# Optimization experiments

Measured on AMD Instinct MI355X. Metric: run time of the kernel, lower is better.

## Reference

```python
import jax, jax.numpy as jnp
import numpy as np

D_MODEL = 1024
NUM_HEADS = 16
HEAD_DIM = D_MODEL // NUM_HEADS
MAX_SEQ_LEN = 2048
THETA = 10000.0
BATCH = 2
SEQ = 2048


def _rope_tables():
    inv_freq = 1.0 / (THETA ** (jnp.arange(0, HEAD_DIM, 2, dtype=jnp.float32) / HEAD_DIM))
    pos = jnp.arange(MAX_SEQ_LEN, dtype=jnp.float32)
    freqs = pos[:, None] * inv_freq[None, :]  # [max_seq, head_dim/2]
    return jnp.sin(freqs), jnp.cos(freqs)


def _apply_rope(x, sin, cos):
    # x: [b, h, s, d]; sin/cos: [s, d/2] -> broadcast over b, h
    sin = sin[None, None, :, :]
    cos = cos[None, None, :, :]
    x_even = x[..., 0::2]
    x_odd = x[..., 1::2]
    out_even = x_even * cos - x_odd * sin
    out_odd = x_even * sin + x_odd * cos
    # interleave back: stack on new last axis then flatten
    out = jnp.stack((out_even, out_odd), axis=-1)
    return out.reshape(x.shape)


def setup_inputs() -> dict:
    key = jax.random.key(0)
    ks = jax.random.split(key, 5)
    std = (2.0 / (D_MODEL + D_MODEL)) ** 0.5
    return {
        "x": jax.random.normal(ks[0], (BATCH, SEQ, D_MODEL), dtype=jnp.float32),
        "Wq": jax.random.normal(ks[1], (D_MODEL, D_MODEL), dtype=jnp.float32) * std,
        "Wk": jax.random.normal(ks[2], (D_MODEL, D_MODEL), dtype=jnp.float32) * std,
        "Wv": jax.random.normal(ks[3], (D_MODEL, D_MODEL), dtype=jnp.float32) * std,
        "Wo": jax.random.normal(ks[4], (D_MODEL, D_MODEL), dtype=jnp.float32) * std,
    }


def reference(x, Wq, Wk, Wv, Wo):
    b, s, _ = x.shape
    # projections: weight stored [out, in] as in the torch Linear
    Q = jnp.einsum('bsd,od->bso', x, Wq)
    K = jnp.einsum('bsd,od->bso', x, Wk)
    V = jnp.einsum('bsd,od->bso', x, Wv)
    # split heads -> [b, h, s, hd]
    def split(t):
        return t.reshape(b, s, NUM_HEADS, HEAD_DIM).transpose(0, 2, 1, 3)
    Q, K, V = split(Q), split(K), split(V)
    sin, cos = _rope_tables()
    sin, cos = sin[:s], cos[:s]
    Q = _apply_rope(Q, sin, cos)
    K = _apply_rope(K, sin, cos)
    scale = 1.0 / jnp.sqrt(jnp.float32(HEAD_DIM))
    scores = jnp.einsum('bhqd,bhkd->bhqk', Q, K)
    causal = jnp.tril(jnp.ones((s, s), dtype=bool))[None, None]
    scores = jnp.where(causal, scores, -jnp.inf) * scale  # -inf * scale stays -inf
    attn = jax.nn.softmax(scores, axis=-1)
    out = jnp.einsum('bhqk,bhkd->bhqd', attn, V)
    out = out.transpose(0, 2, 1, 3).reshape(b, s, D_MODEL)
    return jnp.einsum('bsd,od->bso', out, Wo)
```

## Files before the change

kernel.cpp:

```cpp
#include <hip/hip_runtime.h>
#include <math.h>

#define NHEADS 16
#define HD 64
#define SEQ 2048
#define BATCH 2
#define DM 1024
#define MTOT (BATCH*SEQ)

typedef __bf16 bf16x8 __attribute__((ext_vector_type(8)));
typedef __bf16 bf16x4 __attribute__((ext_vector_type(4)));
typedef float  f32x4  __attribute__((ext_vector_type(4)));

#define LOG2E 1.4426950408889634f

#define GLD16(gp, lp) __builtin_amdgcn_global_load_lds( \
    (const __attribute__((address_space(1))) void*)(gp), \
    (__attribute__((address_space(3))) void*)(lp), 16, 0, 0)

__global__ __launch_bounds__(256)
void cast_all(const float* __restrict__ x, const float* __restrict__ Wq,
              const float* __restrict__ Wk, const float* __restrict__ Wv,
              const float* __restrict__ Wo,
              __bf16* __restrict__ xb, __bf16* __restrict__ Wqkvb,
              __bf16* __restrict__ Wob)
{
    const size_t NX = (size_t)MTOT * DM;
    const size_t NW_ = (size_t)DM * DM;
    const size_t i = ((size_t)blockIdx.x * 256 + threadIdx.x) * 8;
    const float* src; __bf16* dst; size_t off;
    if (i < NX)               { src = x;  dst = xb;            off = i; }
    else if (i < NX + NW_)    { src = Wq; dst = Wqkvb;         off = i - NX; }
    else if (i < NX + 2*NW_)  { src = Wk; dst = Wqkvb + NW_;   off = i - NX - NW_; }
    else if (i < NX + 3*NW_)  { src = Wv; dst = Wqkvb + 2*NW_; off = i - NX - 2*NW_; }
    else                      { src = Wo; dst = Wob;           off = i - NX - 3*NW_; }
    const float4 f0 = *(const float4*)&src[off];
    const float4 f1 = *(const float4*)&src[off + 4];
    bf16x8 o;
    o[0] = (__bf16)f0.x; o[1] = (__bf16)f0.y; o[2] = (__bf16)f0.z; o[3] = (__bf16)f0.w;
    o[4] = (__bf16)f1.x; o[5] = (__bf16)f1.y; o[6] = (__bf16)f1.z; o[7] = (__bf16)f1.w;
    *(bf16x8*)&dst[off] = o;
}

template<int BM, int BN, int MODE>
__global__ __launch_bounds__(256, 3)
void gemm_mfma(const __bf16* __restrict__ A, const __bf16* __restrict__ W,
               float* __restrict__ Cf,
               __bf16* __restrict__ Qb, __bf16* __restrict__ Kb,
               __bf16* __restrict__ Vtb)
{
    constexpr int IT = BM / 32;
    constexpr int JT = BN / 32;
    __shared__ __bf16 As[BM * 64];
    __shared__ __bf16 Bs[BN * 64];

    const int tid  = threadIdx.x;
    const int lane = tid & 63;
    const int wave = tid >> 6;
    const int ll   = lane & 15;
    const int quad = lane >> 4;
    const int wm   = (wave & 1) * (BM / 2);
    const int wn   = (wave >> 1) * (BN / 2);
    const int bm   = blockIdx.x * BM;
    const int bn   = blockIdx.y * BN;

    const __bf16* Ab = A + (size_t)bm * DM;
    const __bf16* Wb = W + (size_t)bn * DM;

    f32x4 acc[IT][JT];
#pragma unroll
    for (int i = 0; i < IT; i++)
#pragma unroll
        for (int j = 0; j < JT; j++) acc[i][j] = (f32x4){0.f, 0.f, 0.f, 0.f};

    for (int k0 = 0; k0 < DM; k0 += 64) {
#pragma unroll
        for (int j = 0; j < BM / 32; j++) {
            const int t = tid + 256 * j;
            const int r = t >> 3, g = t & 7;
            GLD16(Ab + (size_t)r * DM + k0 + ((g ^ (r & 7)) * 8), &As[t * 8]);
        }
#pragma unroll
        for (int j = 0; j < BN / 32; j++) {
            const int t = tid + 256 * j;
            const int r = t >> 3, g = t & 7;
            GLD16(Wb + (size_t)r * DM + k0 + ((g ^ (r & 7)) * 8), &Bs[t * 8]);
        }
        __syncthreads();

#pragma unroll
        for (int kh = 0; kh < 2; kh++) {
            bf16x8 af[IT], bfr[JT];
#pragma unroll
            for (int i = 0; i < IT; i++) {
                const int r = wm + i*16 + ll;
                const int g = kh*4 + quad;
                af[i] = *(const bf16x8*)&As[(r*8 + (g ^ (r & 7))) * 8];
            }
#pragma unroll
            for (int j = 0; j < JT; j++) {
                const int r = wn + j*16 + ll;
                const int g = kh*4 + quad;
                bfr[j] = *(const bf16x8*)&Bs[(r*8 + (g ^ (r & 7))) * 8];
            }
#pragma unroll
            for (int i = 0; i < IT; i++)
#pragma unroll
                for (int j = 0; j < JT; j++)
                    acc[i][j] = __builtin_amdgcn_mfma_f32_16x16x32_bf16(
                        af[i], bfr[j], acc[i][j], 0, 0, 0);
        }
        __syncthreads();
    }

    if (MODE == 1) {
#pragma unroll
        for (int i = 0; i < IT; i++) {
#pragma unroll
            for (int j = 0; j < JT; j++) {
                const int gc = bn + wn + j*16 + ll;
#pragma unroll
                for (int r = 0; r < 4; r++) {
                    const int gr = bm + wm + i*16 + quad*4 + r;
                    Cf[(size_t)gr * DM + gc] = acc[i][j][r];
                }
            }
        }
    } else {
        const int which = bn >> 10;
        const int nb = bn & 1023;
#pragma unroll
        for (int i = 0; i < IT; i++) {
            const int m0 = bm + wm + i*16 + quad*4;
            const int b  = m0 >> 11;
            const int s0 = m0 & (SEQ - 1);
#pragma unroll
            for (int j = 0; j < JT; j++) {
                const int n_g = nb + wn + j*16 + ll;
                const int h = n_g >> 6, d = n_g & (HD - 1);
                if (which == 2) {
                    bf16x4 pk;
#pragma unroll
                    for (int r = 0; r < 4; r++) pk[r] = (__bf16)acc[i][j][r];
                    *(bf16x4*)&Vtb[((size_t)((b*NHEADS + h)*HD + d)) * SEQ + s0] = pk;
                } else {
                    __bf16* P = (which == 0) ? Qb : Kb;
                    const float sc = (which == 0) ? 0.125f * LOG2E : 1.0f;
                    const float inv =
                        exp2f(-(float)(d & ~1) * (13.287712379549449f / 64.0f));
                    const bool odd = (d & 1);
#pragma unroll
                    for (int r = 0; r < 4; r++) {
                        const float own = acc[i][j][r];
                        const float oth = __shfl_xor(own, 1);
                        float sn, cs;
                        __sincosf((float)(s0 + r) * inv, &sn, &cs);
                        const float xe = odd ? oth : own;
                        const float xo = odd ? own : oth;
                        const float o = odd ? (xe * sn + xo * cs)
                                            : (xe * cs - xo * sn);
                        P[((size_t)(b*NHEADS + h) * SEQ + s0 + r) * HD + d] =
                            (__bf16)(o * sc);
                    }
                }
            }
        }
    }
}

__global__ __launch_bounds__(256, 2)
void attn_mfma(const __bf16* __restrict__ Qb, const __bf16* __restrict__ Kb,
               const __bf16* __restrict__ Vtb, __bf16* __restrict__ AOb)
{
    __shared__ __align__(16) __bf16 ptB[4][16][64];
    __shared__ float comb[4][64][17];
    __shared__ float lbuf[4][64];

    const int tid  = threadIdx.x;
    const int wave = tid >> 6;
    const int lane = tid & 63;
    const int m    = lane & 15;
    const int quad = lane >> 4;
    const int bh   = blockIdx.x;
    const int b    = bh >> 4, h = bh & 15;
    const int qb   = blockIdx.z ? (SEQ/64 - 1) - (int)blockIdx.y : (int)blockIdx.y;
    const int q0   = qb * 64;

    const __bf16* Qp = Qb + (size_t)bh * SEQ * HD;
    const __bf16* Kp = Kb + (size_t)bh * SEQ * HD;
    const __bf16* Vp = Vtb + (size_t)bh * HD * SEQ;

    bf16x8 ones;
#pragma unroll
    for (int j = 0; j < 8; j++) ones[j] = (__bf16)1.0f;

    bf16x8 qf[4][2];
#pragma unroll
    for (int i = 0; i < 4; i++) {
        const __bf16* qp = Qp + (size_t)(q0 + i*16 + m) * HD + quad*8;
        qf[i][0] = *(const bf16x8*)qp;
        qf[i][1] = *(const bf16x8*)(qp + 32);
    }

    f32x4 acc[4][4];
    f32x4 l_acc[4];
#pragma unroll
    for (int i = 0; i < 4; i++) {
        l_acc[i] = (f32x4){0.f, 0.f, 0.f, 0.f};
#pragma unroll
        for (int nt = 0; nt < 4; nt++) acc[i][nt] = (f32x4){0.f, 0.f, 0.f, 0.f};
    }

    for (int t = wave; t <= qb; t += 4) {
        const int k0 = t * 64;
        const bool diag = (t == qb);

        bf16x8 kf[4][2], vf[4][2];
#pragma unroll
        for (int tk = 0; tk < 4; tk++) {
            const __bf16* kp = Kp + (size_t)(k0 + tk*16 + m) * HD + quad*8;
            kf[tk][0] = *(const bf16x8*)kp;
            kf[tk][1] = *(const bf16x8*)(kp + 32);
            const __bf16* vp = Vp + (size_t)(tk*16 + m) * SEQ + k0 + quad*8;
            vf[tk][0] = *(const bf16x8*)vp;
            vf[tk][1] = *(const bf16x8*)(vp + 32);
        }

#pragma unroll
        for (int i = 0; i < 4; i++) {
            f32x4 s[4];
#pragma unroll
            for (int tk = 0; tk < 4; tk++) {
                s[tk] = (f32x4){0.f, 0.f, 0.f, 0.f};
                s[tk] = __builtin_amdgcn_mfma_f32_16x16x32_bf16(
                    kf[tk][0], qf[i][0], s[tk], 0, 0, 0);
                s[tk] = __builtin_amdgcn_mfma_f32_16x16x32_bf16(
                    kf[tk][1], qf[i][1], s[tk], 0, 0, 0);
            }
#pragma unroll
            for (int tk = 0; tk < 4; tk++) {
                bf16x4 pk;
#pragma unroll
                for (int r = 0; r < 4; r++) {
                    float sv = s[tk][r];
                    if (diag)
                        sv = (16*tk + quad*4 + r <= 16*i + m) ? sv : -INFINITY;
                    pk[r] = (__bf16)__builtin_amdgcn_exp2f(sv);
                }
                const int Gs = (2*tk + (quad >> 1)) ^ (m & 7);
                *(bf16x4*)&ptB[wave][m][Gs*8 + (quad & 1)*4] = pk;
            }
            const bf16x8 af0 =
                *(const bf16x8*)&ptB[wave][m][(quad ^ (m & 7))*8];
            const bf16x8 af1 =
                *(const bf16x8*)&ptB[wave][m][((4 + quad) ^ (m & 7))*8];
            l_acc[i] = __builtin_amdgcn_mfma_f32_16x16x32_bf16(
                af0, ones, l_acc[i], 0, 0, 0);
            l_acc[i] = __builtin_amdgcn_mfma_f32_16x16x32_bf16(
                af1, ones, l_acc[i], 0, 0, 0);
#pragma unroll
            for (int nt = 0; nt < 4; nt++) {
                acc[i][nt] = __builtin_amdgcn_mfma_f32_16x16x32_bf16(
                    af0, vf[nt][0], acc[i][nt], 0, 0, 0);
                acc[i][nt] = __builtin_amdgcn_mfma_f32_16x16x32_bf16(
                    af1, vf[nt][1], acc[i][nt], 0, 0, 0);
            }
        }
    }

    if (m == 0) {
#pragma unroll
        for (int i = 0; i < 4; i++)
#pragma unroll
            for (int r = 0; r < 4; r++)
                lbuf[wave][i*16 + quad*4 + r] = l_acc[i][r];
    }
    __syncthreads();

    const int row = tid >> 2;
    const int c0  = (tid & 3) * 4;
    const float rl = 1.0f / (lbuf[0][row] + lbuf[1][row]
                           + lbuf[2][row] + lbuf[3][row]);
    __bf16* op = AOb + (size_t)(b * SEQ + q0 + row) * DM + h * HD;

#pragma unroll
    for (int nt = 0; nt < 4; nt++) {
#pragma unroll
        for (int i = 0; i < 4; i++)
#pragma unroll
            for (int r = 0; r < 4; r++)
                comb[wave][i*16 + quad*4 + r][m] = acc[i][nt][r];
        __syncthreads();
        bf16x4 ov;
#pragma unroll
        for (int cc = 0; cc < 4; cc++) {
            const int col = c0 + cc;
            const float o = comb[0][row][col] + comb[1][row][col]
                          + comb[2][row][col] + comb[3][row][col];
            ov[cc] = (__bf16)(o * rl);
        }
        *(bf16x4*)&op[nt*16 + c0] = ov;
        if (nt < 3) __syncthreads();
    }
}

extern "C" void kernel_launch(void* const* d_in, const int* in_sizes, int n_in,
                              void* d_out, int out_size, void* d_ws, size_t ws_size,
                              hipStream_t stream) {
    const float* x  = (const float*)d_in[0];
    const float* Wq = (const float*)d_in[1];
    const float* Wk = (const float*)d_in[2];
    const float* Wv = (const float*)d_in[3];
    const float* Wo = (const float*)d_in[4];
    float* out = (float*)d_out;

    char* ws = (char*)d_ws;
    __bf16* xb    = (__bf16*)ws;
    __bf16* Wqkvb = (__bf16*)(ws + ((size_t)8  << 20));
    __bf16* Wob   = (__bf16*)(ws + ((size_t)14 << 20));
    __bf16* Qb    = (__bf16*)(ws + ((size_t)16 << 20));
    __bf16* Kb    = (__bf16*)(ws + ((size_t)24 << 20));
    __bf16* Vtb   = (__bf16*)(ws + ((size_t)32 << 20));
    __bf16* AOb   = (__bf16*)(ws + ((size_t)40 << 20));

    cast_all<<<4096, 256, 0, stream>>>(x, Wq, Wk, Wv, Wo, xb, Wqkvb, Wob);

    gemm_mfma<128,128,0><<<dim3(MTOT/128, 3072/128), 256, 0, stream>>>(
        xb, Wqkvb, nullptr, Qb, Kb, Vtb);

    attn_mfma<<<dim3(BATCH*NHEADS, SEQ/128, 2), 256, 0, stream>>>(
        Qb, Kb, Vtb, AOb);

    gemm_mfma<128,128,1><<<dim3(MTOT/128, DM/128), 256, 0, stream>>>(
        AOb, Wob, out, nullptr, nullptr, nullptr);
}
```

Measured before the change: 171.7 us.

## Rewrite attention inner loop with 32x32x16 MFMA and register-resident P

The attention kernel now uses 32x32x16 bf16 MFMA tiles instead of 16x16x32. The score accumulator layout lets exp'd probabilities be packed straight into the A operand of the PV MFMA, with no LDS round trip through ptB. Row sums are computed with scalar adds in place of the ones-vector MFMA. Fully masked upper sub-tiles on the diagonal block are skipped, and the epilogue reduction is reorganized around the new layout. The cost is more register pressure from the 16-wide accumulators, plus extra syncs in the epilogue.

```diff
diff --git a/kernel.cpp b/kernel.cpp
--- a/kernel.cpp
+++ b/kernel.cpp
@@ -10,7 +10,10 @@
 
 typedef __bf16 bf16x8 __attribute__((ext_vector_type(8)));
 typedef __bf16 bf16x4 __attribute__((ext_vector_type(4)));
+typedef __bf16 bf16x2 __attribute__((ext_vector_type(2)));
 typedef float  f32x4  __attribute__((ext_vector_type(4)));
+typedef float  f32x16 __attribute__((ext_vector_type(16)));
+typedef unsigned u32x4 __attribute__((ext_vector_type(4)));
 
 #define LOG2E 1.4426950408889634f
 
@@ -168,19 +171,23 @@
     }
 }
 
+static __device__ __forceinline__ unsigned pk2(float a, float b) {
+    bf16x2 t; t[0] = (__bf16)a; t[1] = (__bf16)b;
+    return __builtin_bit_cast(unsigned, t);
+}
+
 __global__ __launch_bounds__(256, 2)
 void attn_mfma(const __bf16* __restrict__ Qb, const __bf16* __restrict__ Kb,
                const __bf16* __restrict__ Vtb, __bf16* __restrict__ AOb)
 {
-    __shared__ __align__(16) __bf16 ptB[4][16][64];
-    __shared__ float comb[4][64][17];
-    __shared__ float lbuf[4][64];
+    __shared__ float comb[4][32][33];
+    __shared__ float lbuf[4][2][64];
 
     const int tid  = threadIdx.x;
     const int wave = tid >> 6;
     const int lane = tid & 63;
-    const int m    = lane & 15;
-    const int quad = lane >> 4;
+    const int col  = lane & 31;
+    const int hi   = lane >> 5;
     const int bh   = blockIdx.x;
     const int b    = bh >> 4, h = bh & 15;
     const int qb   = blockIdx.z ? (SEQ/64 - 1) - (int)blockIdx.y : (int)blockIdx.y;
@@ -190,117 +197,121 @@
     const __bf16* Kp = Kb + (size_t)bh * SEQ * HD;
     const __bf16* Vp = Vtb + (size_t)bh * HD * SEQ;
 
-    bf16x8 ones;
-#pragma unroll
-    for (int j = 0; j < 8; j++) ones[j] = (__bf16)1.0f;
-
-    bf16x8 qf[4][2];
-#pragma unroll
-    for (int i = 0; i < 4; i++) {
-        const __bf16* qp = Qp + (size_t)(q0 + i*16 + m) * HD + quad*8;
-        qf[i][0] = *(const bf16x8*)qp;
-        qf[i][1] = *(const bf16x8*)(qp + 32);
-    }
-
-    f32x4 acc[4][4];
-    f32x4 l_acc[4];
-#pragma unroll
-    for (int i = 0; i < 4; i++) {
-        l_acc[i] = (f32x4){0.f, 0.f, 0.f, 0.f};
-#pragma unroll
-        for (int nt = 0; nt < 4; nt++) acc[i][nt] = (f32x4){0.f, 0.f, 0.f, 0.f};
-    }
+    bf16x8 qf[2][4];
+#pragma unroll
+    for (int i = 0; i < 2; i++)
+#pragma unroll
+        for (int c = 0; c < 4; c++)
+            qf[i][c] = *(const bf16x8*)&Qp[(size_t)(q0 + 32*i + col) * HD
+                                           + 16*c + 8*hi];
+
+    f32x16 acc[2][2];
+#pragma unroll
+    for (int i = 0; i < 2; i++)
+#pragma unroll
+        for (int dt = 0; dt < 2; dt++) acc[i][dt] = (f32x16){};
+    float lsum[2] = {0.f, 0.f};
+
+    const int cr = col - 4*hi;
 
     for (int t = wave; t <= qb; t += 4) {
         const int k0 = t * 64;
         const bool diag = (t == qb);
 
-        bf16x8 kf[4][2], vf[4][2];
-#pragma unroll
-        for (int tk = 0; tk < 4; tk++) {
-            const __bf16* kp = Kp + (size_t)(k0 + tk*16 + m) * HD + quad*8;
-            kf[tk][0] = *(const bf16x8*)kp;
-            kf[tk][1] = *(const bf16x8*)(kp + 32);
-            const __bf16* vp = Vp + (size_t)(tk*16 + m) * SEQ + k0 + quad*8;
-            vf[tk][0] = *(const bf16x8*)vp;
-            vf[tk][1] = *(const bf16x8*)(vp + 32);
-        }
-
-#pragma unroll
-        for (int i = 0; i < 4; i++) {
-            f32x4 s[4];
-#pragma unroll
-            for (int tk = 0; tk < 4; tk++) {
-                s[tk] = (f32x4){0.f, 0.f, 0.f, 0.f};
-                s[tk] = __builtin_amdgcn_mfma_f32_16x16x32_bf16(
-                    kf[tk][0], qf[i][0], s[tk], 0, 0, 0);
-                s[tk] = __builtin_amdgcn_mfma_f32_16x16x32_bf16(
-                    kf[tk][1], qf[i][1], s[tk], 0, 0, 0);
-            }
-#pragma unroll
-            for (int tk = 0; tk < 4; tk++) {
-                bf16x4 pk;
-#pragma unroll
-                for (int r = 0; r < 4; r++) {
-                    float sv = s[tk][r];
-                    if (diag)
-                        sv = (16*tk + quad*4 + r <= 16*i + m) ? sv : -INFINITY;
-                    pk[r] = (__bf16)__builtin_amdgcn_exp2f(sv);
+        bf16x8 kf[2][4];
+#pragma unroll
+        for (int kt = 0; kt < 2; kt++)
+#pragma unroll
+            for (int c = 0; c < 4; c++)
+                kf[kt][c] = *(const bf16x8*)&Kp[(size_t)(k0 + 32*kt + col) * HD
+                                                + 16*c + 8*hi];
+        bf16x4 vf[2][4][2];
+#pragma unroll
+        for (int dt = 0; dt < 2; dt++)
+#pragma unroll
+            for (int c = 0; c < 4; c++) {
+                const __bf16* vrow = &Vp[(size_t)(32*dt + col) * SEQ + k0 + 16*c];
+                vf[dt][c][0] = *(const bf16x4*)(vrow + 4*hi);
+                vf[dt][c][1] = *(const bf16x4*)(vrow + 8 + 4*hi);
+            }
+
+#pragma unroll
+        for (int i = 0; i < 2; i++) {
+#pragma unroll
+            for (int kt = 0; kt < 2; kt++) {
+                if (kt > i && diag) continue;
+                f32x16 s = (f32x16){};
+#pragma unroll
+                for (int c = 0; c < 4; c++)
+                    s = __builtin_amdgcn_mfma_f32_32x32x16_bf16(
+                        kf[kt][c], qf[i][c], s, 0, 0, 0);
+                const bool tri = diag && (kt == i);
+                float p[16];
+#pragma unroll
+                for (int r = 0; r < 16; r++) {
+                    float sv = s[r];
+                    if (tri && ((r & 3) + 8*(r >> 2) > cr)) sv = -INFINITY;
+                    p[r] = __builtin_amdgcn_exp2f(sv);
                 }
-                const int Gs = (2*tk + (quad >> 1)) ^ (m & 7);
-                *(bf16x4*)&ptB[wave][m][Gs*8 + (quad & 1)*4] = pk;
-            }
-            const bf16x8 af0 =
-                *(const bf16x8*)&ptB[wave][m][(quad ^ (m & 7))*8];
-            const bf16x8 af1 =
-                *(const bf16x8*)&ptB[wave][m][((4 + quad) ^ (m & 7))*8];
-            l_acc[i] = __builtin_amdgcn_mfma_f32_16x16x32_bf16(
-                af0, ones, l_acc[i], 0, 0, 0);
-            l_acc[i] = __builtin_amdgcn_mfma_f32_16x16x32_bf16(
-                af1, ones, l_acc[i], 0, 0, 0);
-#pragma unroll
-            for (int nt = 0; nt < 4; nt++) {
-                acc[i][nt] = __builtin_amdgcn_mfma_f32_16x16x32_bf16(
-                    af0, vf[nt][0], acc[i][nt], 0, 0, 0);
-                acc[i][nt] = __builtin_amdgcn_mfma_f32_16x16x32_bf16(
-                    af1, vf[nt][1], acc[i][nt], 0, 0, 0);
+                float ls = ((p[0]+p[1])+(p[2]+p[3])) + ((p[4]+p[5])+(p[6]+p[7]))
+                         + ((p[8]+p[9])+(p[10]+p[11])) + ((p[12]+p[13])+(p[14]+p[15]));
+                lsum[i] += ls;
+                const u32x4 w0 = {pk2(p[0],  p[1]),  pk2(p[2],  p[3]),
+                                  pk2(p[4],  p[5]),  pk2(p[6],  p[7])};
+                const u32x4 w1 = {pk2(p[8],  p[9]),  pk2(p[10], p[11]),
+                                  pk2(p[12], p[13]), pk2(p[14], p[15])};
+                const bf16x8 a0 = __builtin_bit_cast(bf16x8, w0);
+                const bf16x8 a1 = __builtin_bit_cast(bf16x8, w1);
+#pragma unroll
+                for (int dt = 0; dt < 2; dt++) {
+                    bf16x8 v0, v1;
+#pragma unroll
+                    for (int e = 0; e < 4; e++) {
+                        v0[e]   = vf[dt][2*kt][0][e];
+                        v0[4+e] = vf[dt][2*kt][1][e];
+                        v1[e]   = vf[dt][2*kt+1][0][e];
+                        v1[4+e] = vf[dt][2*kt+1][1][e];
+                    }
+                    acc[i][dt] = __builtin_amdgcn_mfma_f32_32x32x16_bf16(
+                        a0, v0, acc[i][dt], 0, 0, 0);
+                    acc[i][dt] = __builtin_amdgcn_mfma_f32_32x32x16_bf16(
+                        a1, v1, acc[i][dt], 0, 0, 0);
+                }
             }
         }
     }
 
-    if (m == 0) {
-#pragma unroll
-        for (int i = 0; i < 4; i++)
-#pragma unroll
-            for (int r = 0; r < 4; r++)
-                lbuf[wave][i*16 + quad*4 + r] = l_acc[i][r];
-    }
+#pragma unroll
+    for (int i = 0; i < 2; i++)
+        lbuf[wave][hi][32*i + col] = lsum[i];
     __syncthreads();
 
-    const int row = tid >> 2;
-    const int c0  = (tid & 3) * 4;
-    const float rl = 1.0f / (lbuf[0][row] + lbuf[1][row]
-                           + lbuf[2][row] + lbuf[3][row]);
-    __bf16* op = AOb + (size_t)(b * SEQ + q0 + row) * DM + h * HD;
-
-#pragma unroll
-    for (int nt = 0; nt < 4; nt++) {
-#pragma unroll
-        for (int i = 0; i < 4; i++)
-#pragma unroll
-            for (int r = 0; r < 4; r++)
-                comb[wave][i*16 + quad*4 + r][m] = acc[i][nt][r];
-        __syncthreads();
-        bf16x4 ov;
-#pragma unroll
-        for (int cc = 0; cc < 4; cc++) {
-            const int col = c0 + cc;
-            const float o = comb[0][row][col] + comb[1][row][col]
-                          + comb[2][row][col] + comb[3][row][col];
-            ov[cc] = (__bf16)(o * rl);
-        }
-        *(bf16x4*)&op[nt*16 + c0] = ov;
-        if (nt < 3) __syncthreads();
+    const int qq  = tid >> 3;
+    const int dd0 = (tid & 7) * 4;
+#pragma unroll
+    for (int i = 0; i < 2; i++) {
+        float lt = 0.f;
+#pragma unroll
+        for (int w = 0; w < 4; w++)
+            lt += lbuf[w][0][32*i + qq] + lbuf[w][1][32*i + qq];
+        const float rl = 1.0f / lt;
+#pragma unroll
+        for (int dt = 0; dt < 2; dt++) {
+#pragma unroll
+            for (int r = 0; r < 16; r++)
+                comb[wave][(r & 3) + 8*(r >> 2) + 4*hi][col] = acc[i][dt][r];
+            __syncthreads();
+            bf16x4 ov;
+#pragma unroll
+            for (int cc = 0; cc < 4; cc++) {
+                const float o = comb[0][qq][dd0+cc] + comb[1][qq][dd0+cc]
+                              + comb[2][qq][dd0+cc] + comb[3][qq][dd0+cc];
+                ov[cc] = (__bf16)(o * rl);
+            }
+            *(bf16x4*)&AOb[(size_t)(b*SEQ + q0 + 32*i + qq) * DM
+                           + h*HD + 32*dt + dd0] = ov;
+            __syncthreads();
+        }
     }
 }
 
```

New measurement: 180.1 us. 4.9% more time.
